# Optimization experiments

Hardware: AMD Instinct MI355X
Metric: run time of the kernel (lower is better)

The kernel has to match this reference:

```python
import jax, jax.numpy as jnp
import numpy as np

B, T, C = 4, 2048, 1024
N_HEAD = 16
HEAD_DIM = C // N_HEAD


def setup_inputs() -> dict:
    key = jax.random.key(0)
    ks = jax.random.split(key, 5)
    scale = 0.02
    return {
        "x": jax.random.normal(ks[0], (B, T, C), dtype=jnp.float32),
        "w_attn": jax.random.normal(ks[1], (C, 3 * C), dtype=jnp.float32) * scale,
        "b_attn": jax.random.normal(ks[2], (3 * C,), dtype=jnp.float32) * scale,
        "w_proj": jax.random.normal(ks[3], (C, C), dtype=jnp.float32) * scale,
        "b_proj": jax.random.normal(ks[4], (C,), dtype=jnp.float32) * scale,
    }


def reference(x, w_attn, b_attn, w_proj, b_proj):
    Bq, Tq, Cq = x.shape
    qkv = x @ w_attn + b_attn  # [B, T, 3C]
    q, k, v = jnp.split(qkv, 3, axis=2)
    # [B, H, T, D]
    q = q.reshape(Bq, Tq, N_HEAD, HEAD_DIM).transpose(0, 2, 1, 3)
    k = k.reshape(Bq, Tq, N_HEAD, HEAD_DIM).transpose(0, 2, 1, 3)
    v = v.reshape(Bq, Tq, N_HEAD, HEAD_DIM).transpose(0, 2, 1, 3)
    att = jnp.einsum("bhqd,bhkd->bhqk", q, k) * (HEAD_DIM ** -0.5)
    causal = jnp.tril(jnp.ones((Tq, Tq), dtype=bool))
    att = jnp.where(causal[None, None, :, :], att, -jnp.inf)
    att = jax.nn.softmax(att, axis=-1)
    out = jnp.einsum("bhqk,bhkd->bhqd", att, v)  # [B, H, T, D]
    out = out.transpose(0, 2, 1, 3).reshape(Bq, Tq, Cq)
    return out @ w_proj + b_proj
```

## Files before the change

kernel.cpp:

```cpp
#include <hip/hip_runtime.h>
#include <hip/hip_bf16.h>

#define Bsz 4
#define Tsz 2048
#define Csz 1024
#define NH  16
#define HD  64
#define NT  (Bsz * Tsz)

typedef unsigned short u16;
typedef unsigned int   u32;
typedef u16   u16x8  __attribute__((ext_vector_type(8)));
typedef u16   u16x4  __attribute__((ext_vector_type(4)));
typedef u32   u32x2  __attribute__((ext_vector_type(2)));
typedef short s16x8  __attribute__((ext_vector_type(8)));
typedef float f32x4  __attribute__((ext_vector_type(4)));

__device__ __forceinline__ float b2f(u16 u) {
    union { unsigned int i; float f; } x; x.i = ((unsigned int)u) << 16; return x.f;
}
__device__ __forceinline__ u16 f2b(float f) {
    unsigned int u = __float_as_uint(f);
    return (u16)((u + 0x7FFF + ((u >> 16) & 1)) >> 16);
}
__device__ __forceinline__ float ex2(float x) {
    float r; asm("v_exp_f32 %0, %1" : "=v"(r) : "v"(x)); return r;
}
__device__ __forceinline__ u32 cvtpk(float lo, float hi) {
    u32 r; asm("v_cvt_pk_bf16_f32 %0, %1, %2" : "=v"(r) : "v"(lo), "v"(hi)); return r;
}
__device__ __forceinline__ void gload16(const u16* g, u16* l) {
    __builtin_amdgcn_global_load_lds(
        (const __attribute__((address_space(1))) void*)g,
        (__attribute__((address_space(3))) void*)l, 16, 0, 0);
}

__global__ __launch_bounds__(256)
void conv_f32_bf16(const float* __restrict__ in, u16* __restrict__ out, int n8)
{
    int t = blockIdx.x * 256 + threadIdx.x;
    if (t >= n8) return;
    const float4* p = reinterpret_cast<const float4*>(in) + (size_t)t * 2;
    float4 a = p[0], b = p[1];
    u16x8 w;
    w[0] = f2b(a.x); w[1] = f2b(a.y); w[2] = f2b(a.z); w[3] = f2b(a.w);
    w[4] = f2b(b.x); w[5] = f2b(b.y); w[6] = f2b(b.z); w[7] = f2b(b.w);
    *(reinterpret_cast<u16x8*>(out) + t) = w;
}

__global__ __launch_bounds__(256)
void transpose_conv(const float* __restrict__ in, u16* __restrict__ out, int K, int N)
{
    __shared__ float tile[32][33];
    const int n0 = blockIdx.x * 32, k0 = blockIdx.y * 32;
    const int tx = threadIdx.x & 31, ty = threadIdx.x >> 5;
#pragma unroll
    for (int j = 0; j < 4; ++j)
        tile[ty + j * 8][tx] = in[(size_t)(k0 + ty + j * 8) * N + n0 + tx];
    __syncthreads();
#pragma unroll
    for (int j = 0; j < 4; ++j)
        out[(size_t)(n0 + ty + j * 8) * K + k0 + tx] = f2b(tile[tx][ty + j * 8]);
}

template<typename OutT>
__global__ __launch_bounds__(256)
void gemm_bf16(const u16* __restrict__ A, const u16* __restrict__ Bt,
               const float* __restrict__ bias, OutT* __restrict__ C,
               int M, int N, int K)
{
    __shared__ u16 As[128 * 64];
    __shared__ u16 Bs[128 * 64];

    const int tid  = threadIdx.x;
    const int lane = tid & 63;
    const int wid  = tid >> 6;
    const int wr   = wid >> 1;
    const int wc   = wid & 1;
    const int g    = lane >> 4;
    const int rr   = lane & 15;
    const int srow = lane >> 3;
    const int sslt = lane & 7;

    const int n0 = blockIdx.x * 128;
    const int m0 = blockIdx.y * 128;

    f32x4 acc[4][4];
#pragma unroll
    for (int m = 0; m < 4; ++m)
#pragma unroll
        for (int n = 0; n < 4; ++n) acc[m][n] = (f32x4){0.f, 0.f, 0.f, 0.f};

    for (int k0 = 0; k0 < K; k0 += 64) {
        __syncthreads();
#pragma unroll
        for (int p = 0; p < 4; ++p) {
            const int q = p * 4 + wid;
            const int r = q * 8 + srow;
            gload16(A  + (size_t)(m0 + r) * K + k0 + sslt * 8, &As[q * 512]);
            gload16(Bt + (size_t)(n0 + r) * K + k0 + sslt * 8, &Bs[q * 512]);
        }
        __syncthreads();

#pragma unroll
        for (int kk = 0; kk < 2; ++kk) {
            s16x8 af[4], bfr[4];
            const int s = kk * 4 + g;
#pragma unroll
            for (int m = 0; m < 4; ++m)
                af[m] = *reinterpret_cast<const s16x8*>(
                    &As[(wr * 64 + m * 16 + rr) * 64 + s * 8]);
#pragma unroll
            for (int n = 0; n < 4; ++n)
                bfr[n] = *reinterpret_cast<const s16x8*>(
                    &Bs[(wc * 64 + n * 16 + rr) * 64 + s * 8]);
#pragma unroll
            for (int m = 0; m < 4; ++m)
#pragma unroll
                for (int n = 0; n < 4; ++n)
                    acc[m][n] = __builtin_amdgcn_mfma_f32_16x16x32_bf16(
                        af[m], bfr[n], acc[m][n], 0, 0, 0);
        }
    }

#pragma unroll
    for (int m = 0; m < 4; ++m) {
#pragma unroll
        for (int n = 0; n < 4; ++n) {
            const int col = n0 + wc * 64 + n * 16 + rr;
            const float bv = bias[col];
#pragma unroll
            for (int j = 0; j < 4; ++j) {
                const int row = m0 + wr * 64 + m * 16 + g * 4 + j;
                const float v = acc[m][n][j] + bv;
                if constexpr (sizeof(OutT) == 2)
                    C[(size_t)row * N + col] = (OutT)f2b(v);
                else
                    C[(size_t)row * N + col] = (OutT)v;
            }
        }
    }
}

__global__ __launch_bounds__(256)
void attn_mfma(const u16* __restrict__ qkv, u16* __restrict__ out)
{
    __shared__ __align__(128) u16 Ks[64 * 64];
    __shared__ __align__(128) u16 Vt[64 * 64];
    __shared__ __align__(128) u16 Pl[4 * 2048];

    const int tid  = threadIdx.x;
    const int lane = tid & 63;
    const int wid  = tid >> 6;
    const int c    = lane & 15;
    const int g    = lane >> 4;

    const int bh = blockIdx.x;
    const int b  = bh >> 4;
    const int h  = bh & 15;
    const int skey = tid >> 3;
    const int sb   = tid & 7;
    const u32 pbyte = ((u32)(size_t)(&Pl[0])) + wid * 4096 + lane * 8;
    const float QSC = 0.18033688f;

    for (int half = 0; half < 2; ++half) {
        const int yt = half ? 15 - (int)blockIdx.y : (int)blockIdx.y;
        const int t0 = yt * 128;
        const int qb0 = t0 + wid * 32;

        s16x8 qf[2][2];
#pragma unroll
        for (int m = 0; m < 2; ++m)
#pragma unroll
            for (int kk = 0; kk < 2; ++kk) {
                u16x8 raw = *reinterpret_cast<const u16x8*>(
                    qkv + (size_t)(b * Tsz + qb0 + m * 16 + c) * (3 * Csz)
                        + h * HD + kk * 32 + g * 8);
                s16x8 qv;
#pragma unroll
                for (int i = 0; i < 8; ++i) qv[i] = (short)f2b(b2f(raw[i]) * QSC);
                qf[m][kk] = qv;
            }

        f32x4 acco[2][4];
#pragma unroll
        for (int m = 0; m < 2; ++m)
#pragma unroll
            for (int dn = 0; dn < 4; ++dn) acco[m][dn] = (f32x4){0.f, 0.f, 0.f, 0.f};
        float mrun[8], lrun[8];
#pragma unroll
        for (int i = 0; i < 8; ++i) { mrun[i] = -1e30f; lrun[i] = 0.f; }

        for (int kt = 0; kt < t0 + 128; kt += 64) {
#pragma unroll
            for (int p = 0; p < 2; ++p) {
                const int key = skey + p * 32;
                const u16* gk = qkv + (size_t)(b * Tsz + kt + key) * (3 * Csz)
                                + Csz + h * HD + sb * 8;
                u16x8 kv = *reinterpret_cast<const u16x8*>(gk);
                u16x8 vv = *reinterpret_cast<const u16x8*>(gk + Csz);
                *reinterpret_cast<u16x8*>(&Ks[key * 64 + ((sb ^ (key & 7)) * 8)]) = kv;
#pragma unroll
                for (int i = 0; i < 8; ++i) {
                    const int d = sb * 8 + i;
                    Vt[d * 64 + (key ^ (((i ^ sb) & 7) << 3))] = vv[i];
                }
            }
            __syncthreads();

            if (kt <= qb0 + 31) {
                f32x4 accS[2][4];
#pragma unroll
                for (int m = 0; m < 2; ++m)
#pragma unroll
                    for (int n = 0; n < 4; ++n) accS[m][n] = (f32x4){0.f, 0.f, 0.f, 0.f};
#pragma unroll
                for (int kk = 0; kk < 2; ++kk) {
                    s16x8 kf[4];
#pragma unroll
                    for (int n = 0; n < 4; ++n) {
                        const int key = n * 16 + c;
                        kf[n] = *reinterpret_cast<const s16x8*>(
                            &Ks[key * 64 + (((kk * 4 + g) ^ (c & 7)) * 8)]);
                    }
#pragma unroll
                    for (int m = 0; m < 2; ++m)
#pragma unroll
                        for (int n = 0; n < 4; ++n)
                            accS[m][n] = __builtin_amdgcn_mfma_f32_16x16x32_bf16(
                                qf[m][kk], kf[n], accS[m][n], 0, 0, 0);
                }

                if (kt + 63 > qb0) {
#pragma unroll
                    for (int m = 0; m < 2; ++m)
#pragma unroll
                        for (int n = 0; n < 4; ++n) {
                            const int kgl = kt + n * 16 + c;
#pragma unroll
                            for (int j = 0; j < 4; ++j) {
                                const int qg = qb0 + m * 16 + g * 4 + j;
                                if (kgl > qg) accS[m][n][j] = -1e30f;
                            }
                        }
                }

                float pm[8];
#pragma unroll
                for (int m = 0; m < 2; ++m)
#pragma unroll
                    for (int j = 0; j < 4; ++j)
                        pm[m * 4 + j] = fmaxf(fmaxf(accS[m][0][j], accS[m][1][j]),
                                              fmaxf(accS[m][2][j], accS[m][3][j]));
#pragma unroll
                for (int msk = 1; msk < 16; msk <<= 1)
#pragma unroll
                    for (int i = 0; i < 8; ++i)
                        pm[i] = fmaxf(pm[i], __shfl_xor(pm[i], msk));

                int need = 0;
#pragma unroll
                for (int i = 0; i < 8; ++i) need |= (pm[i] > mrun[i] + 8.f);
                if (__any(need)) {
                    float cvec[8];
#pragma unroll
                    for (int i = 0; i < 8; ++i) {
                        const float mn = fmaxf(mrun[i], pm[i]);
                        cvec[i] = ex2(mrun[i] - mn);
                        mrun[i] = mn;
                        lrun[i] *= cvec[i];
                    }
#pragma unroll
                    for (int m = 0; m < 2; ++m)
#pragma unroll
                        for (int dn = 0; dn < 4; ++dn)
#pragma unroll
                            for (int j = 0; j < 4; ++j)
                                acco[m][dn][j] *= cvec[m * 4 + j];
                }

#pragma unroll
                for (int m = 0; m < 2; ++m)
#pragma unroll
                    for (int n = 0; n < 4; ++n) {
                        float pv[4];
#pragma unroll
                        for (int j = 0; j < 4; ++j) {
                            pv[j] = ex2(accS[m][n][j] - mrun[m * 4 + j]);
                            lrun[m * 4 + j] += pv[j];
                        }
                        const u32 w0 = cvtpk(pv[0], pv[1]);
                        const u32 w1 = cvtpk(pv[2], pv[3]);
                        const int slot = (n >> 1) * 32 + ((c >> 2) & 1) * 16
                                       + ((n & 1) * 2 + (c >> 3)) * 4 + (c & 3);
                        *reinterpret_cast<u32x2*>(
                            &Pl[wid * 2048 + m * 1024 + slot * 16 + g * 4]) = (u32x2){w0, w1};
                    }
                asm volatile("s_waitcnt lgkmcnt(0)" ::: "memory");
                __builtin_amdgcn_sched_barrier(0);

                u16x4 t000, t001, t010, t011, t100, t101, t110, t111;
                asm volatile("ds_read_b64_tr_b16 %0, %1"             : "=v"(t000) : "v"(pbyte));
                asm volatile("ds_read_b64_tr_b16 %0, %1 offset:512"  : "=v"(t001) : "v"(pbyte));
                asm volatile("ds_read_b64_tr_b16 %0, %1 offset:1024" : "=v"(t010) : "v"(pbyte));
                asm volatile("ds_read_b64_tr_b16 %0, %1 offset:1536" : "=v"(t011) : "v"(pbyte));
                asm volatile("ds_read_b64_tr_b16 %0, %1 offset:2048" : "=v"(t100) : "v"(pbyte));
                asm volatile("ds_read_b64_tr_b16 %0, %1 offset:2560" : "=v"(t101) : "v"(pbyte));
                asm volatile("ds_read_b64_tr_b16 %0, %1 offset:3072" : "=v"(t110) : "v"(pbyte));
                asm volatile("ds_read_b64_tr_b16 %0, %1 offset:3584" : "=v"(t111) : "v"(pbyte));
                asm volatile("s_waitcnt lgkmcnt(0)" ::: "memory");
                __builtin_amdgcn_sched_barrier(0);

                s16x8 pa[2][2];
#pragma unroll
                for (int q = 0; q < 4; ++q) {
                    pa[0][0][q] = (short)t000[q]; pa[0][0][q + 4] = (short)t001[q];
                    pa[0][1][q] = (short)t010[q]; pa[0][1][q + 4] = (short)t011[q];
                    pa[1][0][q] = (short)t100[q]; pa[1][0][q + 4] = (short)t101[q];
                    pa[1][1][q] = (short)t110[q]; pa[1][1][q + 4] = (short)t111[q];
                }

#pragma unroll
                for (int kk = 0; kk < 2; ++kk) {
                    s16x8 vf[4];
#pragma unroll
                    for (int dn = 0; dn < 4; ++dn) {
                        const int d = dn * 16 + c;
                        const int swz = (c & 7) ^ ((dn * 2 + (c >> 3)) & 7);
                        vf[dn] = *reinterpret_cast<const s16x8*>(
                            &Vt[d * 64 + (((kk * 4 + g) ^ swz) * 8)]);
                    }
#pragma unroll
                    for (int m = 0; m < 2; ++m)
#pragma unroll
                        for (int dn = 0; dn < 4; ++dn)
                            acco[m][dn] = __builtin_amdgcn_mfma_f32_16x16x32_bf16(
                                pa[m][kk], vf[dn], acco[m][dn], 0, 0, 0);
                }
            }
            __syncthreads();
        }

#pragma unroll
        for (int msk = 1; msk < 16; msk <<= 1)
#pragma unroll
            for (int i = 0; i < 8; ++i)
                lrun[i] += __shfl_xor(lrun[i], msk);
        float inv[8];
#pragma unroll
        for (int i = 0; i < 8; ++i) inv[i] = 1.f / lrun[i];
#pragma unroll
        for (int m = 0; m < 2; ++m)
#pragma unroll
            for (int dn = 0; dn < 4; ++dn)
#pragma unroll
                for (int j = 0; j < 4; ++j) {
                    const int q = qb0 + m * 16 + g * 4 + j;
                    out[(size_t)(b * Tsz + q) * Csz + h * HD + dn * 16 + c] =
                        f2b(acco[m][dn][j] * inv[m * 4 + j]);
                }
    }
}

extern "C" void kernel_launch(void* const* d_in, const int* in_sizes, int n_in,
                              void* d_out, int out_size, void* d_ws, size_t ws_size,
                              hipStream_t stream) {
    const float* x      = (const float*)d_in[0];
    const float* w_attn = (const float*)d_in[1];
    const float* b_attn = (const float*)d_in[2];
    const float* w_proj = (const float*)d_in[3];
    const float* b_proj = (const float*)d_in[4];
    float* out = (float*)d_out;

    char* w = (char*)d_ws;
    u16* qkv_bf = (u16*)w;  w += (size_t)NT * 3 * Csz * 2;
    u16* x_bf   = (u16*)w;  w += (size_t)NT * Csz * 2;
    u16* ao_bf  = (u16*)w;  w += (size_t)NT * Csz * 2;
    u16* wat    = (u16*)w;  w += (size_t)3 * Csz * Csz * 2;
    u16* wpt    = (u16*)w;

    conv_f32_bf16<<<(NT * Csz / 8 + 255) / 256, 256, 0, stream>>>(x, x_bf, NT * Csz / 8);
    transpose_conv<<<dim3(3 * Csz / 32, Csz / 32), 256, 0, stream>>>(w_attn, wat, Csz, 3 * Csz);
    transpose_conv<<<dim3(Csz / 32, Csz / 32), 256, 0, stream>>>(w_proj, wpt, Csz, Csz);

    gemm_bf16<u16><<<dim3(3 * Csz / 128, NT / 128), 256, 0, stream>>>(
        x_bf, wat, b_attn, qkv_bf, NT, 3 * Csz, Csz);

    attn_mfma<<<dim3(Bsz * NH, 8), 256, 0, stream>>>(qkv_bf, ao_bf);

    gemm_bf16<float><<<dim3(Csz / 128, NT / 128), 256, 0, stream>>>(
        ao_bf, wpt, b_proj, out, NT, Csz, Csz);
}
```

Baseline: 299.9 us.

## Shrink attention query tile to 64 rows and double the grid

The attention kernel now has each block process 64 query rows (16 per wave) instead of 128, and the grid doubles along y to 16 paired tiles. This gives twice as many blocks and less wasted causal work per block, with fewer registers and less P scratch in shared memory. The change also moves the barrier to the top of the loop and adds s_setprio around the MFMA sections. In exchange, each K/V tile loaded into shared memory now feeds half as many query rows, so global and LDS load traffic per unit of compute roughly doubles.

```diff
diff --git a/kernel.cpp b/kernel.cpp
--- a/kernel.cpp
+++ b/kernel.cpp
@@ -34,6 +34,15 @@
         (const __attribute__((address_space(1))) void*)g,
         (__attribute__((address_space(3))) void*)l, 16, 0, 0);
 }
+__device__ __forceinline__ void tr4(u32 a, u16x4 t[4]) {
+    asm volatile("ds_read_b64_tr_b16 %0, %1"             : "=v"(t[0]) : "v"(a));
+    asm volatile("ds_read_b64_tr_b16 %0, %1 offset:512"  : "=v"(t[1]) : "v"(a));
+    asm volatile("ds_read_b64_tr_b16 %0, %1 offset:1024" : "=v"(t[2]) : "v"(a));
+    asm volatile("ds_read_b64_tr_b16 %0, %1 offset:1536" : "=v"(t[3]) : "v"(a));
+}
+#define LGKM0_FENCE() do { \
+    asm volatile("s_waitcnt lgkmcnt(0)" ::: "memory"); \
+    __builtin_amdgcn_sched_barrier(0); } while (0)
 
 __global__ __launch_bounds__(256)
 void conv_f32_bf16(const float* __restrict__ in, u16* __restrict__ out, int n8)
@@ -147,7 +156,7 @@
 {
     __shared__ __align__(128) u16 Ks[64 * 64];
     __shared__ __align__(128) u16 Vt[64 * 64];
-    __shared__ __align__(128) u16 Pl[4 * 2048];
+    __shared__ __align__(128) u16 Pl[4 * 1024];
 
     const int tid  = threadIdx.x;
     const int lane = tid & 63;
@@ -158,40 +167,39 @@
     const int bh = blockIdx.x;
     const int b  = bh >> 4;
     const int h  = bh & 15;
+
     const int skey = tid >> 3;
     const int sb   = tid & 7;
-    const u32 pbyte = ((u32)(size_t)(&Pl[0])) + wid * 4096 + lane * 8;
+    const int kswz = (sb ^ (skey & 7)) * 8;
+    const int slotc = ((c >> 2) & 1) * 16 + (c >> 3) * 4 + (c & 3);
+    const u32 pbyte = ((u32)(size_t)(&Pl[0])) + wid * 2048 + lane * 8;
     const float QSC = 0.18033688f;
 
     for (int half = 0; half < 2; ++half) {
-        const int yt = half ? 15 - (int)blockIdx.y : (int)blockIdx.y;
-        const int t0 = yt * 128;
-        const int qb0 = t0 + wid * 32;
-
-        s16x8 qf[2][2];
-#pragma unroll
-        for (int m = 0; m < 2; ++m)
-#pragma unroll
-            for (int kk = 0; kk < 2; ++kk) {
-                u16x8 raw = *reinterpret_cast<const u16x8*>(
-                    qkv + (size_t)(b * Tsz + qb0 + m * 16 + c) * (3 * Csz)
-                        + h * HD + kk * 32 + g * 8);
-                s16x8 qv;
-#pragma unroll
-                for (int i = 0; i < 8; ++i) qv[i] = (short)f2b(b2f(raw[i]) * QSC);
-                qf[m][kk] = qv;
-            }
-
-        f32x4 acco[2][4];
-#pragma unroll
-        for (int m = 0; m < 2; ++m)
-#pragma unroll
-            for (int dn = 0; dn < 4; ++dn) acco[m][dn] = (f32x4){0.f, 0.f, 0.f, 0.f};
-        float mrun[8], lrun[8];
-#pragma unroll
-        for (int i = 0; i < 8; ++i) { mrun[i] = -1e30f; lrun[i] = 0.f; }
-
-        for (int kt = 0; kt < t0 + 128; kt += 64) {
+        const int yt  = half ? 31 - (int)blockIdx.y : (int)blockIdx.y;
+        const int t0  = yt * 64;
+        const int qb0 = t0 + wid * 16;
+
+        s16x8 qf[2];
+#pragma unroll
+        for (int kk = 0; kk < 2; ++kk) {
+            u16x8 raw = *reinterpret_cast<const u16x8*>(
+                qkv + (size_t)(b * Tsz + qb0 + c) * (3 * Csz) + h * HD + kk * 32 + g * 8);
+            s16x8 qv;
+#pragma unroll
+            for (int i = 0; i < 8; ++i) qv[i] = (short)f2b(b2f(raw[i]) * QSC);
+            qf[kk] = qv;
+        }
+
+        f32x4 acco[4];
+#pragma unroll
+        for (int dn = 0; dn < 4; ++dn) acco[dn] = (f32x4){0.f, 0.f, 0.f, 0.f};
+        float mrun[4], lrun[4];
+#pragma unroll
+        for (int i = 0; i < 4; ++i) { mrun[i] = -1e30f; lrun[i] = 0.f; }
+
+        for (int kt = 0; kt <= t0; kt += 64) {
+            __syncthreads();
 #pragma unroll
             for (int p = 0; p < 2; ++p) {
                 const int key = skey + p * 32;
@@ -199,7 +207,7 @@
                                 + Csz + h * HD + sb * 8;
                 u16x8 kv = *reinterpret_cast<const u16x8*>(gk);
                 u16x8 vv = *reinterpret_cast<const u16x8*>(gk + Csz);
-                *reinterpret_cast<u16x8*>(&Ks[key * 64 + ((sb ^ (key & 7)) * 8)]) = kv;
+                *reinterpret_cast<u16x8*>(&Ks[key * 64 + kswz]) = kv;
 #pragma unroll
                 for (int i = 0; i < 8; ++i) {
                     const int d = sb * 8 + i;
@@ -208,157 +216,127 @@
             }
             __syncthreads();
 
-            if (kt <= qb0 + 31) {
-                f32x4 accS[2][4];
-#pragma unroll
-                for (int m = 0; m < 2; ++m)
-#pragma unroll
-                    for (int n = 0; n < 4; ++n) accS[m][n] = (f32x4){0.f, 0.f, 0.f, 0.f};
-#pragma unroll
-                for (int kk = 0; kk < 2; ++kk) {
-                    s16x8 kf[4];
-#pragma unroll
-                    for (int n = 0; n < 4; ++n) {
-                        const int key = n * 16 + c;
-                        kf[n] = *reinterpret_cast<const s16x8*>(
-                            &Ks[key * 64 + (((kk * 4 + g) ^ (c & 7)) * 8)]);
-                    }
-#pragma unroll
-                    for (int m = 0; m < 2; ++m)
-#pragma unroll
-                        for (int n = 0; n < 4; ++n)
-                            accS[m][n] = __builtin_amdgcn_mfma_f32_16x16x32_bf16(
-                                qf[m][kk], kf[n], accS[m][n], 0, 0, 0);
-                }
-
-                if (kt + 63 > qb0) {
-#pragma unroll
-                    for (int m = 0; m < 2; ++m)
-#pragma unroll
-                        for (int n = 0; n < 4; ++n) {
-                            const int kgl = kt + n * 16 + c;
-#pragma unroll
-                            for (int j = 0; j < 4; ++j) {
-                                const int qg = qb0 + m * 16 + g * 4 + j;
-                                if (kgl > qg) accS[m][n][j] = -1e30f;
-                            }
-                        }
-                }
-
-                float pm[8];
-#pragma unroll
-                for (int m = 0; m < 2; ++m)
+            f32x4 accS[4];
+#pragma unroll
+            for (int n = 0; n < 4; ++n) accS[n] = (f32x4){0.f, 0.f, 0.f, 0.f};
+            __builtin_amdgcn_s_setprio(1);
+#pragma unroll
+            for (int kk = 0; kk < 2; ++kk) {
+                s16x8 kf[4];
+#pragma unroll
+                for (int n = 0; n < 4; ++n) {
+                    const int key = n * 16 + c;
+                    kf[n] = *reinterpret_cast<const s16x8*>(
+                        &Ks[key * 64 + (((kk * 4 + g) ^ (c & 7)) * 8)]);
+                }
+#pragma unroll
+                for (int n = 0; n < 4; ++n)
+                    accS[n] = __builtin_amdgcn_mfma_f32_16x16x32_bf16(
+                        qf[kk], kf[n], accS[n], 0, 0, 0);
+            }
+            __builtin_amdgcn_s_setprio(0);
+
+            if (kt == t0) {
+#pragma unroll
+                for (int n = 0; n < 4; ++n) {
+                    const int kgl = kt + n * 16 + c;
 #pragma unroll
                     for (int j = 0; j < 4; ++j)
-                        pm[m * 4 + j] = fmaxf(fmaxf(accS[m][0][j], accS[m][1][j]),
-                                              fmaxf(accS[m][2][j], accS[m][3][j]));
-#pragma unroll
-                for (int msk = 1; msk < 16; msk <<= 1)
-#pragma unroll
-                    for (int i = 0; i < 8; ++i)
-                        pm[i] = fmaxf(pm[i], __shfl_xor(pm[i], msk));
-
-                int need = 0;
-#pragma unroll
-                for (int i = 0; i < 8; ++i) need |= (pm[i] > mrun[i] + 8.f);
-                if (__any(need)) {
-                    float cvec[8];
-#pragma unroll
-                    for (int i = 0; i < 8; ++i) {
-                        const float mn = fmaxf(mrun[i], pm[i]);
-                        cvec[i] = ex2(mrun[i] - mn);
-                        mrun[i] = mn;
-                        lrun[i] *= cvec[i];
-                    }
-#pragma unroll
-                    for (int m = 0; m < 2; ++m)
-#pragma unroll
-                        for (int dn = 0; dn < 4; ++dn)
-#pragma unroll
-                            for (int j = 0; j < 4; ++j)
-                                acco[m][dn][j] *= cvec[m * 4 + j];
-                }
-
-#pragma unroll
-                for (int m = 0; m < 2; ++m)
-#pragma unroll
-                    for (int n = 0; n < 4; ++n) {
-                        float pv[4];
-#pragma unroll
-                        for (int j = 0; j < 4; ++j) {
-                            pv[j] = ex2(accS[m][n][j] - mrun[m * 4 + j]);
-                            lrun[m * 4 + j] += pv[j];
-                        }
-                        const u32 w0 = cvtpk(pv[0], pv[1]);
-                        const u32 w1 = cvtpk(pv[2], pv[3]);
-                        const int slot = (n >> 1) * 32 + ((c >> 2) & 1) * 16
-                                       + ((n & 1) * 2 + (c >> 3)) * 4 + (c & 3);
-                        *reinterpret_cast<u32x2*>(
-                            &Pl[wid * 2048 + m * 1024 + slot * 16 + g * 4]) = (u32x2){w0, w1};
-                    }
-                asm volatile("s_waitcnt lgkmcnt(0)" ::: "memory");
-                __builtin_amdgcn_sched_barrier(0);
-
-                u16x4 t000, t001, t010, t011, t100, t101, t110, t111;
-                asm volatile("ds_read_b64_tr_b16 %0, %1"             : "=v"(t000) : "v"(pbyte));
-                asm volatile("ds_read_b64_tr_b16 %0, %1 offset:512"  : "=v"(t001) : "v"(pbyte));
-                asm volatile("ds_read_b64_tr_b16 %0, %1 offset:1024" : "=v"(t010) : "v"(pbyte));
-                asm volatile("ds_read_b64_tr_b16 %0, %1 offset:1536" : "=v"(t011) : "v"(pbyte));
-                asm volatile("ds_read_b64_tr_b16 %0, %1 offset:2048" : "=v"(t100) : "v"(pbyte));
-                asm volatile("ds_read_b64_tr_b16 %0, %1 offset:2560" : "=v"(t101) : "v"(pbyte));
-                asm volatile("ds_read_b64_tr_b16 %0, %1 offset:3072" : "=v"(t110) : "v"(pbyte));
-                asm volatile("ds_read_b64_tr_b16 %0, %1 offset:3584" : "=v"(t111) : "v"(pbyte));
-                asm volatile("s_waitcnt lgkmcnt(0)" ::: "memory");
-                __builtin_amdgcn_sched_barrier(0);
-
-                s16x8 pa[2][2];
+                        if (kgl > qb0 + g * 4 + j) accS[n][j] = -1e30f;
+                }
+            }
+
+            float pm[4];
+#pragma unroll
+            for (int j = 0; j < 4; ++j)
+                pm[j] = fmaxf(fmaxf(accS[0][j], accS[1][j]),
+                              fmaxf(accS[2][j], accS[3][j]));
+#pragma unroll
+            for (int msk = 1; msk < 16; msk <<= 1)
+#pragma unroll
+                for (int i = 0; i < 4; ++i)
+                    pm[i] = fmaxf(pm[i], __shfl_xor(pm[i], msk));
+
+            int need = 0;
+#pragma unroll
+            for (int i = 0; i < 4; ++i) need |= (pm[i] > mrun[i] + 8.f);
+            if (__any(need)) {
+                float cv[4];
+#pragma unroll
+                for (int i = 0; i < 4; ++i) {
+                    const float mn = fmaxf(mrun[i], pm[i]);
+                    cv[i] = ex2(mrun[i] - mn);
+                    mrun[i] = mn;
+                    lrun[i] *= cv[i];
+                }
+#pragma unroll
+                for (int dn = 0; dn < 4; ++dn)
+#pragma unroll
+                    for (int j = 0; j < 4; ++j)
+                        acco[dn][j] *= cv[j];
+            }
+
+#pragma unroll
+            for (int n = 0; n < 4; ++n) {
+                float pv[4];
+#pragma unroll
+                for (int j = 0; j < 4; ++j) {
+                    pv[j] = ex2(accS[n][j] - mrun[j]);
+                    lrun[j] += pv[j];
+                }
+                const int slot = (n >> 1) * 32 + (n & 1) * 8 + slotc;
+                *reinterpret_cast<u32x2*>(&Pl[wid * 1024 + slot * 16 + g * 4]) =
+                    (u32x2){cvtpk(pv[0], pv[1]), cvtpk(pv[2], pv[3])};
+            }
+            LGKM0_FENCE();
+
+            u16x4 tp[4];
+            tr4(pbyte, tp);
+            LGKM0_FENCE();
+            s16x8 pa[2];
+#pragma unroll
+            for (int kk = 0; kk < 2; ++kk)
 #pragma unroll
                 for (int q = 0; q < 4; ++q) {
-                    pa[0][0][q] = (short)t000[q]; pa[0][0][q + 4] = (short)t001[q];
-                    pa[0][1][q] = (short)t010[q]; pa[0][1][q + 4] = (short)t011[q];
-                    pa[1][0][q] = (short)t100[q]; pa[1][0][q + 4] = (short)t101[q];
-                    pa[1][1][q] = (short)t110[q]; pa[1][1][q + 4] = (short)t111[q];
-                }
-
-#pragma unroll
-                for (int kk = 0; kk < 2; ++kk) {
-                    s16x8 vf[4];
-#pragma unroll
-                    for (int dn = 0; dn < 4; ++dn) {
-                        const int d = dn * 16 + c;
-                        const int swz = (c & 7) ^ ((dn * 2 + (c >> 3)) & 7);
-                        vf[dn] = *reinterpret_cast<const s16x8*>(
-                            &Vt[d * 64 + (((kk * 4 + g) ^ swz) * 8)]);
-                    }
-#pragma unroll
-                    for (int m = 0; m < 2; ++m)
-#pragma unroll
-                        for (int dn = 0; dn < 4; ++dn)
-                            acco[m][dn] = __builtin_amdgcn_mfma_f32_16x16x32_bf16(
-                                pa[m][kk], vf[dn], acco[m][dn], 0, 0, 0);
-                }
-            }
-            __syncthreads();
+                    pa[kk][q]     = (short)tp[kk * 2][q];
+                    pa[kk][q + 4] = (short)tp[kk * 2 + 1][q];
+                }
+
+#pragma unroll
+            for (int kk = 0; kk < 2; ++kk) {
+                s16x8 vf[4];
+#pragma unroll
+                for (int dn = 0; dn < 4; ++dn) {
+                    const int d = dn * 16 + c;
+                    const int swz = (c & 7) ^ ((dn * 2 + (c >> 3)) & 7);
+                    vf[dn] = *reinterpret_cast<const s16x8*>(
+                        &Vt[d * 64 + (((kk * 4 + g) ^ swz) * 8)]);
+                }
+                __builtin_amdgcn_s_setprio(1);
+#pragma unroll
+                for (int dn = 0; dn < 4; ++dn)
+                    acco[dn] = __builtin_amdgcn_mfma_f32_16x16x32_bf16(
+                        pa[kk], vf[dn], acco[dn], 0, 0, 0);
+                __builtin_amdgcn_s_setprio(0);
+            }
         }
 
 #pragma unroll
         for (int msk = 1; msk < 16; msk <<= 1)
 #pragma unroll
-            for (int i = 0; i < 8; ++i)
+            for (int i = 0; i < 4; ++i)
                 lrun[i] += __shfl_xor(lrun[i], msk);
-        float inv[8];
-#pragma unroll
-        for (int i = 0; i < 8; ++i) inv[i] = 1.f / lrun[i];
-#pragma unroll
-        for (int m = 0; m < 2; ++m)
-#pragma unroll
-            for (int dn = 0; dn < 4; ++dn)
-#pragma unroll
-                for (int j = 0; j < 4; ++j) {
-                    const int q = qb0 + m * 16 + g * 4 + j;
-                    out[(size_t)(b * Tsz + q) * Csz + h * HD + dn * 16 + c] =
-                        f2b(acco[m][dn][j] * inv[m * 4 + j]);
-                }
+        float inv[4];
+#pragma unroll
+        for (int i = 0; i < 4; ++i) inv[i] = 1.f / lrun[i];
+#pragma unroll
+        for (int dn = 0; dn < 4; ++dn)
+#pragma unroll
+            for (int j = 0; j < 4; ++j) {
+                const int q = qb0 + g * 4 + j;
+                out[(size_t)(b * Tsz + q) * Csz + h * HD + dn * 16 + c] =
+                    f2b(acco[dn][j] * inv[j]);
+            }
     }
 }
 
@@ -386,7 +364,7 @@
     gemm_bf16<u16><<<dim3(3 * Csz / 128, NT / 128), 256, 0, stream>>>(
         x_bf, wat, b_attn, qkv_bf, NT, 3 * Csz, Csz);
 
-    attn_mfma<<<dim3(Bsz * NH, 8), 256, 0, stream>>>(qkv_bf, ao_bf);
+    attn_mfma<<<dim3(Bsz * NH, 16), 256, 0, stream>>>(qkv_bf, ao_bf);
 
     gemm_bf16<float><<<dim3(Csz / 128, NT / 128), 256, 0, stream>>>(
         ao_bf, wpt, b_proj, out, NT, Csz, Csz);
```

New measurement: 316.1 us. +5.4%, slower.
